# Kernel optimization log

Hardware: AMD Instinct MI355X
Metric: run time of the kernel (lower is better)

Reference implementation:

```python
import jax, jax.numpy as jnp
import numpy as np

KDIM = 2048
RATE = 0.99

def _l2norm(v, axis=1, eps=1e-12):
    n = jnp.linalg.norm(v, axis=axis, keepdims=True)
    return v / jnp.maximum(n, eps)

def _conv3d(x, w, b, stride, pad):
    # x: (N,C,D,H,W), w: (O,I,kd,kh,kw)
    out = jax.lax.conv_general_dilated(
        x, w, window_strides=stride, padding=pad,
        dimension_numbers=('NCDHW', 'OIDHW', 'NCDHW'))
    return out + b[None, :, None, None, None]

def _linear(x, w, b):
    # torch Linear convention: w (out,in)
    return x @ w.T + b

def _memory_block(x, m):
    # x: (n, 400), m: (k, 400)
    k = m.shape[0]
    xn = _l2norm(x)
    mn = _l2norm(m)
    score = xn @ mn.T                                  # (n, k)
    # --- EMA codebook update (fully detached) ---
    xd = jax.lax.stop_gradient(x)
    ind = jnp.argmax(score, axis=1)                    # (n,)
    onehot_sum = jax.ops.segment_sum(jnp.ones(x.shape[0], x.dtype), ind, num_segments=k)
    embed_sum = jax.ops.segment_sum(xd, ind, num_segments=k).T   # (c, k)
    embed_mean = embed_sum / (onehot_sum + 1e-6)                 # (c, k)
    ss = embed_mean.sum(axis=1, keepdims=True)                   # (c, 1)
    param_div = (embed_mean - ss) * 2.0 / k / (k - 1)
    m_new = jax.lax.stop_gradient(m * RATE + (embed_mean + param_div).T * (1.0 - RATE))
    # --- recompute score with updated codebook ---
    mn = _l2norm(m_new)
    score = xn @ mn.T
    out = score @ m_new                                 # (n, c)
    tend = jnp.linalg.norm(out, axis=1)
    tend_1 = jnp.linalg.norm(x, axis=1)
    param = (tend_1 / tend)[:, None]
    out = (param * score) @ m_new
    return out, score


def setup_inputs() -> dict:
    key = jax.random.key(0)
    ks = jax.random.split(key, 24)
    f32 = jnp.float32
    def rn(k, shape, scale):
        return jax.random.normal(k, shape, dtype=f32) * scale
    b = 2048
    inp = {
        'x': rn(ks[0], (b, 1, 200, 5, 5), 1.0),
        'conv1_w': rn(ks[1], (20, 1, 3, 3, 3), 0.2),   'conv1_b': jnp.zeros((20,), f32),
        'pool1_w': rn(ks[2], (20, 20, 3, 1, 1), 0.1),  'pool1_b': jnp.zeros((20,), f32),
        'conv2_w': rn(ks[3], (35, 20, 3, 3, 3), 0.05), 'conv2_b': jnp.zeros((35,), f32),
        'pool2_w': rn(ks[4], (35, 35, 3, 1, 1), 0.1),  'pool2_b': jnp.zeros((35,), f32),
        'conv3_w': rn(ks[5], (35, 35, 3, 1, 1), 0.1),  'conv3_b': jnp.zeros((35,), f32),
        'conv4_w': rn(ks[6], (35, 35, 2, 1, 1), 0.1),  'conv4_b': jnp.zeros((35,), f32),
        'feat_w':  rn(ks[7], (400, 910), 0.03),        'feat_b': jnp.zeros((400,), f32),
        'feat1_w': rn(ks[8], (400, 400), 0.05),        'feat1_b': jnp.zeros((400,), f32),
        'mem_units': rn(ks[9], (KDIM, 400), 1.0),
        'up_w':    rn(ks[10], (400, 400), 0.05),       'up_b': jnp.zeros((400,), f32),
        'cls_w':   rn(ks[11], (16, 400), 0.05),        'cls_b': jnp.zeros((16,), f32),
    }
    return inp


def reference(x, conv1_w, conv1_b, pool1_w, pool1_b, conv2_w, conv2_b,
              pool2_w, pool2_b, conv3_w, conv3_b, conv4_w, conv4_b,
              feat_w, feat_b, feat1_w, feat1_b, mem_units,
              up_w, up_b, cls_w, cls_b):
    h = jax.nn.relu(_conv3d(x, conv1_w, conv1_b, (1, 1, 1), [(0, 0), (0, 0), (0, 0)]))
    h = _conv3d(h, pool1_w, pool1_b, (2, 1, 1), [(1, 1), (0, 0), (0, 0)])
    h = jax.nn.relu(_conv3d(h, conv2_w, conv2_b, (1, 1, 1), [(1, 1), (0, 0), (0, 0)]))
    h = _conv3d(h, pool2_w, pool2_b, (2, 1, 1), [(1, 1), (0, 0), (0, 0)])
    h = jax.nn.relu(_conv3d(h, conv3_w, conv3_b, (1, 1, 1), [(1, 1), (0, 0), (0, 0)]))
    h = jax.nn.relu(_conv3d(h, conv4_w, conv4_b, (2, 1, 1), [(1, 1), (0, 0), (0, 0)]))
    h = h.reshape(h.shape[0], -1)                 # (b, 910)
    fea = _linear(h, feat_w, feat_b)              # (b, 400)
    xx = _linear(fea, feat1_w, feat1_b)           # (b, 400)
    mem_out, _score = _memory_block(xx, jax.lax.stop_gradient(mem_units))
    up = _linear(mem_out, up_w, up_b)
    out_feature = fea - up
    logits = _linear(out_feature, cls_w, cls_b)   # (b, 16)
    return logits
```

## Files before the change

kernel.cpp:

```cpp
#include <hip/hip_runtime.h>

#define BLK 256

constexpr int BB   = 2048;
constexpr int CH2  = 512;
constexpr int NCH2 = BB / CH2;
constexpr int KD   = 2048;
constexpr int CD   = 400;

__global__ __launch_bounds__(256) void fused12_k(const float* __restrict__ x,
                                                 const float* __restrict__ c1w,
                                                 const float* __restrict__ c1b,
                                                 const float* __restrict__ p1w,
                                                 const float* __restrict__ p1b,
                                                 float* __restrict__ h2c, int b0) {
    int bi = blockIdx.x;
    int o0 = blockIdx.y * 17;
    int ocnt = 99 - o0; if (ocnt > 17) ocnt = 17;
    __shared__ float xs[37 * 25];
    __shared__ float c1[20][35][9];
    __shared__ float w1s[540];
    __shared__ float wps[1200];
    __shared__ float b1s[20], bps[20];
    int tid = threadIdx.x;
    for (int i = tid; i < 540; i += 256) w1s[i] = c1w[i];
    for (int i = tid; i < 1200; i += 256) wps[i] = p1w[i];
    if (tid < 20) { b1s[tid] = c1b[tid]; bps[tid] = p1b[tid]; }
    const float* xb = x + (size_t)(b0 + bi) * 5000;
    int r0 = 2 * o0 - 1;
    for (int i = tid; i < 37 * 25; i += 256) {
        int r = r0 + i / 25;
        xs[i] = (r >= 0 && r < 200) ? xb[r * 25 + (i % 25)] : 0.f;
    }
    __syncthreads();
    for (int it = tid; it < 35 * 5; it += 256) {
        int ri = it / 5, g = it % 5;
        int oc0 = g * 4;
        int r = r0 + ri;
        float acc[4][9];
        if (r >= 0 && r <= 197) {
#pragma unroll
            for (int o = 0; o < 4; ++o)
#pragma unroll
                for (int j = 0; j < 9; ++j) acc[o][j] = b1s[oc0 + o];
#pragma unroll
            for (int kd = 0; kd < 3; ++kd) {
                float xv[25];
                const float* xr = &xs[(ri + kd) * 25];
#pragma unroll
                for (int m = 0; m < 25; ++m) xv[m] = xr[m];
#pragma unroll
                for (int o = 0; o < 4; ++o) {
                    const float* wp1 = &w1s[(oc0 + o) * 27 + kd * 9];
#pragma unroll
                    for (int kh = 0; kh < 3; ++kh)
#pragma unroll
                        for (int kw = 0; kw < 3; ++kw) {
                            float w = wp1[kh * 3 + kw];
#pragma unroll
                            for (int oh = 0; oh < 3; ++oh)
#pragma unroll
                                for (int ow = 0; ow < 3; ++ow)
                                    acc[o][oh * 3 + ow] += xv[(oh + kh) * 5 + ow + kw] * w;
                        }
                }
            }
#pragma unroll
            for (int o = 0; o < 4; ++o)
#pragma unroll
                for (int j = 0; j < 9; ++j) c1[oc0 + o][ri][j] = fmaxf(acc[o][j], 0.f);
        } else {
#pragma unroll
            for (int o = 0; o < 4; ++o)
#pragma unroll
                for (int j = 0; j < 9; ++j) c1[oc0 + o][ri][j] = 0.f;
        }
    }
    __syncthreads();
    for (int it = tid; it < ocnt * 5; it += 256) {
        int oi = it / 5, g = it % 5;
        int oc0 = g * 4;
        float acc[4][9];
#pragma unroll
        for (int o = 0; o < 4; ++o)
#pragma unroll
            for (int j = 0; j < 9; ++j) acc[o][j] = bps[oc0 + o];
        for (int ic = 0; ic < 20; ++ic) {
            float win[3][9];
#pragma unroll
            for (int kd = 0; kd < 3; ++kd)
#pragma unroll
                for (int j = 0; j < 9; ++j) win[kd][j] = c1[ic][2 * oi + kd][j];
#pragma unroll
            for (int o = 0; o < 4; ++o) {
                const float* wp = &wps[((oc0 + o) * 20 + ic) * 3];
#pragma unroll
                for (int kd = 0; kd < 3; ++kd) {
                    float w = wp[kd];
#pragma unroll
                    for (int j = 0; j < 9; ++j) acc[o][j] += win[kd][j] * w;
                }
            }
        }
#pragma unroll
        for (int o = 0; o < 4; ++o) {
            float* ou = h2c + (((size_t)bi * 20 + (oc0 + o)) * 99 + (o0 + oi)) * 9;
#pragma unroll
            for (int j = 0; j < 9; ++j) ou[j] = acc[o][j];
        }
    }
}

__global__ __launch_bounds__(512) void conv2b_k(const float* __restrict__ h2c,
                                                const float* __restrict__ w,
                                                const float* __restrict__ bias,
                                                float* __restrict__ h3, int b0) {
    int bi = blockIdx.x;
    __shared__ float h2s[10][101][9];
    __shared__ float ws[35 * 271];
    int tid = threadIdx.x;
    int oc = tid % 35, run = tid / 35;
    int od_start = run * 7;
    bool active = tid < 490;
    float acc[8];
    float bv = active ? bias[oc] : 0.f;
#pragma unroll
    for (int i = 0; i < 8; ++i) acc[i] = bv;
    const float* src = h2c + (size_t)bi * 17820;
    for (int s = 0; s < 2; ++s) {
        for (int i = tid; i < 10 * 9; i += 512) {
            int ic = i / 9, j = i % 9;
            h2s[ic][0][j] = 0.f; h2s[ic][100][j] = 0.f;
        }
        for (int i = tid; i < 8910; i += 512) {
            int ic = i / 891;
            ((float*)h2s)[i + ic * 18 + 9] = src[s * 8910 + i];
        }
        for (int i = tid; i < 35 * 270; i += 512) {
            int o = i / 270, t = i % 270;
            ws[o * 271 + t] = w[(size_t)o * 540 + s * 270 + t];
        }
        __syncthreads();
        if (active) {
            const float* wp = &ws[oc * 271];
            for (int ic = 0; ic < 10; ++ic) {
#pragma unroll
                for (int j = 0; j < 9; ++j) {
                    float win[10];
#pragma unroll
                    for (int t = 0; t < 10; ++t) win[t] = h2s[ic][od_start + t][j];
#pragma unroll
                    for (int kd = 0; kd < 3; ++kd) {
                        float wv = wp[(ic * 3 + kd) * 9 + j];
#pragma unroll
                        for (int i = 0; i < 8; ++i) acc[i] += win[i + kd] * wv;
                    }
                }
            }
        }
        __syncthreads();
    }
    if (active) {
        float* o = h3 + ((size_t)(b0 + bi) * 35 + oc) * 99 + od_start;
#pragma unroll
        for (int i = 0; i < 8; ++i) o[i] = fmaxf(acc[i], 0.f);
    }
}

__global__ __launch_bounds__(256) void fused345_k(const float* __restrict__ h3,
                                                  const float* __restrict__ w2, const float* __restrict__ b2,
                                                  const float* __restrict__ w3, const float* __restrict__ b3,
                                                  const float* __restrict__ w4, const float* __restrict__ b4,
                                                  float* __restrict__ h6) {
    int b = blockIdx.x;
    __shared__ float h3s[35][101];
    __shared__ float h4s[35][53];
    __shared__ float h5s[35][53];
    __shared__ float wbuf[3675];
    __shared__ float bbuf[35];
    int tid = threadIdx.x;
    int oc = tid % 35, run = tid / 35;
    bool act = tid < 245;
    for (int i = tid; i < 35; i += 256) {
        h3s[i][0] = 0.f; h3s[i][100] = 0.f;
        h4s[i][0] = 0.f; h4s[i][51] = 0.f;
        h5s[i][0] = 0.f; h5s[i][51] = 0.f;
    }
    for (int i = tid; i < 35 * 99; i += 256) h3s[i / 99][1 + i % 99] = h3[(size_t)b * 3465 + i];
    for (int i = tid; i < 3675; i += 256) wbuf[i] = w2[i];
    if (tid < 35) bbuf[tid] = b2[tid];
    __syncthreads();
    if (act) {
        int od0 = run * 7;
        float acc[8];
        float bv = bbuf[oc];
#pragma unroll
        for (int i = 0; i < 8; ++i) acc[i] = bv;
        const float* wrow = &wbuf[oc * 105];
        for (int ic = 0; ic < 35; ++ic) {
            float w0 = wrow[ic * 3], w1 = wrow[ic * 3 + 1], w2v = wrow[ic * 3 + 2];
            float win[17];
#pragma unroll
            for (int t = 0; t < 17; ++t) win[t] = h3s[ic][2 * od0 + t];
#pragma unroll
            for (int i = 0; i < 8; ++i)
                acc[i] += win[2 * i] * w0 + win[2 * i + 1] * w1 + win[2 * i + 2] * w2v;
        }
#pragma unroll
        for (int i = 0; i < 8; ++i) h4s[oc][1 + od0 + i] = acc[i];
    }
    __syncthreads();
    for (int i = tid; i < 3675; i += 256) wbuf[i] = w3[i];
    if (tid < 35) bbuf[tid] = b3[tid];
    __syncthreads();
    if (act) {
        int od0 = run * 7;
        float acc[8];
        float bv = bbuf[oc];
#pragma unroll
        for (int i = 0; i < 8; ++i) acc[i] = bv;
        const float* wrow = &wbuf[oc * 105];
        for (int ic = 0; ic < 35; ++ic) {
            float w0 = wrow[ic * 3], w1 = wrow[ic * 3 + 1], w2v = wrow[ic * 3 + 2];
            float win[10];
#pragma unroll
            for (int t = 0; t < 10; ++t) win[t] = h4s[ic][od0 + t];
#pragma unroll
            for (int i = 0; i < 8; ++i)
                acc[i] += win[i] * w0 + win[i + 1] * w1 + win[i + 2] * w2v;
        }
#pragma unroll
        for (int i = 0; i < 8; ++i) h5s[oc][1 + od0 + i] = fmaxf(acc[i], 0.f);
    }
    __syncthreads();
    for (int i = tid; i < 2450; i += 256) wbuf[i] = w4[i];
    if (tid < 35) bbuf[tid] = b4[tid];
    __syncthreads();
    if (act) {
        int od0 = run * 4; if (od0 > 22) od0 = 22;
        float acc[4];
        float bv = bbuf[oc];
#pragma unroll
        for (int i = 0; i < 4; ++i) acc[i] = bv;
        const float* wrow = &wbuf[oc * 70];
        for (int ic = 0; ic < 35; ++ic) {
            float w0 = wrow[ic * 2], w1 = wrow[ic * 2 + 1];
            float win[8];
#pragma unroll
            for (int t = 0; t < 8; ++t) win[t] = h5s[ic][2 * od0 + t];
#pragma unroll
            for (int i = 0; i < 4; ++i)
                acc[i] += win[2 * i] * w0 + win[2 * i + 1] * w1;
        }
#pragma unroll
        for (int i = 0; i < 4; ++i) {
            int od = od0 + i;
            if (od < 26) h6[(size_t)b * 910 + oc * 26 + od] = fmaxf(acc[i], 0.f);
        }
    }
}

template <int BM, int BN, int TM, int TN, bool GUARD, bool ARGMAX, bool SPLITK>
__global__ __launch_bounds__(256) void gemm_nt(const float* __restrict__ A,
                                               const float* __restrict__ B,
                                               const float* __restrict__ bias,
                                               float* __restrict__ C,
                                               const float* __restrict__ colscale,
                                               unsigned long long* __restrict__ keymax,
                                               int M, int N, int K) {
    constexpr int BK = 16;
    constexpr int AI = BM / 16, BI = BN / 16;
    __shared__ float As[BK][BM + 4];
    __shared__ float Bs[BK][BN + 4];
    int tid = threadIdx.x;
    int tx = tid % (BN / TN), ty = tid / (BN / TN);
    int row0 = blockIdx.y * BM;
    int col0 = blockIdx.x * BN;
    int kbase = 0, kend = K;
    if constexpr (SPLITK) {
        int nz = gridDim.z;
        int kchunk = (((K + nz - 1) / nz) + BK - 1) / BK * BK;
        kbase = blockIdx.z * kchunk;
        kend = kbase + kchunk;
        if (kend > K) kend = K;
    }
    int kk = tid % 16, ld = tid / 16;
    float ra[AI], rb[BI];
    auto loadA = [&](int k0, float* r) {
        int gk = k0 + kk;
#pragma unroll
        for (int i = 0; i < AI; ++i) {
            int gr = row0 + ld + 16 * i;
            float v = 0.f;
            if ((!GUARD && !SPLITK) || (gr < M && gk < kend)) v = A[(size_t)gr * K + gk];
            r[i] = v;
        }
    };
    auto loadB = [&](int k0, float* r) {
        int gk = k0 + kk;
#pragma unroll
        for (int i = 0; i < BI; ++i) {
            int gn = col0 + ld + 16 * i;
            float v = 0.f;
            if ((!GUARD && !SPLITK) || (gn < N && gk < kend)) v = B[(size_t)gn * K + gk];
            r[i] = v;
        }
    };
    auto stash = [&]() {
#pragma unroll
        for (int i = 0; i < AI; ++i) As[kk][ld + 16 * i] = ra[i];
#pragma unroll
        for (int i = 0; i < BI; ++i) Bs[kk][ld + 16 * i] = rb[i];
    };
    float acc[TM][TN] = {};
    int nt = (kend - kbase + BK - 1) / BK;
    loadA(kbase, ra); loadB(kbase, rb);
    stash();
    __syncthreads();
    for (int t = 0; t < nt; ++t) {
        bool more = (t + 1 < nt);
        if (more) { loadA(kbase + (t + 1) * BK, ra); loadB(kbase + (t + 1) * BK, rb); }
#pragma unroll
        for (int k = 0; k < BK; ++k) {
            float a[TM], b[TN];
            *(float4*)&a[0] = *(const float4*)&As[k][ty * TM];
            if constexpr (TM == 8) *(float4*)&a[4] = *(const float4*)&As[k][ty * TM + 4];
            *(float4*)&b[0] = *(const float4*)&Bs[k][tx * TN];
            if constexpr (TN == 8) *(float4*)&b[4] = *(const float4*)&Bs[k][tx * TN + 4];
#pragma unroll
            for (int i = 0; i < TM; ++i)
#pragma unroll
                for (int j = 0; j < TN; ++j) acc[i][j] += a[i] * b[j];
        }
        if (more) {
            __syncthreads();
            stash();
            __syncthreads();
        }
    }
    if constexpr (ARGMAX) {
        __shared__ unsigned long long red[BM][17];
#pragma unroll
        for (int i = 0; i < TM; ++i) {
            unsigned long long best = 0;
#pragma unroll
            for (int j = 0; j < TN; ++j) {
                int gc = col0 + tx * TN + j;
                float v = acc[i][j] * colscale[gc];
                unsigned u = __float_as_uint(v);
                unsigned ukey = (u & 0x80000000u) ? ~u : (u | 0x80000000u);
                unsigned long long key =
                    ((unsigned long long)ukey << 32) | (unsigned)(N - 1 - gc);
                if (key > best) best = key;
            }
            red[ty * TM + i][tx] = best;
        }
        __syncthreads();
        if (tid < BM) {
            unsigned long long best = 0;
#pragma unroll
            for (int q = 0; q < 16; ++q) {
                unsigned long long v = red[tid][q];
                if (v > best) best = v;
            }
            atomicMax(&keymax[row0 + tid], best);
        }
    } else {
#pragma unroll
        for (int i = 0; i < TM; ++i) {
            int gr = row0 + ty * TM + i;
            if (GUARD && gr >= M) continue;
#pragma unroll
            for (int j = 0; j < TN; ++j) {
                int gc = col0 + tx * TN + j;
                if (GUARD && gc >= N) continue;
                float v = acc[i][j];
                if constexpr (SPLITK) {
                    if (bias && blockIdx.z == 0) v += bias[gc];
                    atomicAdd(&C[(size_t)gr * N + gc], v);
                } else {
                    if (bias) v += bias[gc];
                    C[(size_t)gr * N + gc] = v;
                }
            }
        }
    }
}

__global__ __launch_bounds__(256) void gemm_tn_g(const float* __restrict__ mnew,
                                                 const float* __restrict__ nrm2,
                                                 float* __restrict__ G, int kchunk) {
    constexpr int BK = 16;
    __shared__ float As[BK][64];
    __shared__ float Bs[BK][64];
    int tid = threadIdx.x;
    int tx = tid % 16, ty = tid / 16;
    int c0 = blockIdx.y * 64, d0 = blockIdx.x * 64;
    int kbase = blockIdx.z * kchunk;
    int cl = tid % 64, kk0 = tid / 64;
    int gc0 = c0 + cl, gd0 = d0 + cl;
    bool cok = gc0 < CD, dok = gd0 < CD;
    float pa[4], pb[4];
    auto ld = [&](int k0) {
#pragma unroll
        for (int i = 0; i < 4; ++i) {
            int gk = k0 + kk0 + 4 * i;
            float s = 1.0f / fmaxf(nrm2[gk], 1e-12f);
            pa[i] = cok ? mnew[(size_t)gk * CD + gc0] * s : 0.f;
            pb[i] = dok ? mnew[(size_t)gk * CD + gd0] : 0.f;
        }
    };
    auto stash = [&]() {
#pragma unroll
        for (int i = 0; i < 4; ++i) {
            As[kk0 + 4 * i][cl] = pa[i];
            Bs[kk0 + 4 * i][cl] = pb[i];
        }
    };
    float acc[4][4] = {};
    int nt = kchunk / BK;
    ld(kbase); stash(); __syncthreads();
    for (int t = 0; t < nt; ++t) {
        bool more = (t + 1 < nt);
        if (more) ld(kbase + (t + 1) * BK);
#pragma unroll
        for (int k = 0; k < BK; ++k) {
            float a[4], b[4];
            *(float4*)&a[0] = *(const float4*)&As[k][ty * 4];
            *(float4*)&b[0] = *(const float4*)&Bs[k][tx * 4];
#pragma unroll
            for (int i = 0; i < 4; ++i)
#pragma unroll
                for (int j = 0; j < 4; ++j) acc[i][j] += a[i] * b[j];
        }
        if (more) { __syncthreads(); stash(); __syncthreads(); }
    }
#pragma unroll
    for (int i = 0; i < 4; ++i) {
        int gc = c0 + ty * 4 + i;
        if (gc >= CD) continue;
#pragma unroll
        for (int j = 0; j < 4; ++j) {
            int gd = d0 + tx * 4 + j;
            if (gd >= CD) continue;
            atomicAdd(&G[(size_t)gc * CD + gd], acc[i][j]);
        }
    }
}


__global__ __launch_bounds__(BLK) void rownorm_k(const float* __restrict__ in,
                                                 float* __restrict__ nrm, int rows, int cols) {
    int row  = blockIdx.x * (BLK / 64) + ((int)threadIdx.x / 64);
    int lane = threadIdx.x & 63;
    if (row >= rows) return;
    const float* p = in + (size_t)row * cols;
    float s = 0.f;
    for (int c = lane; c < cols; c += 64) { float v = p[c]; s += v * v; }
#pragma unroll
    for (int off = 32; off; off >>= 1) s += __shfl_down(s, off);
    if (lane == 0) nrm[row] = sqrtf(s);
}

__global__ __launch_bounds__(BLK) void scatter_k(const float* __restrict__ xx,
                                                 const unsigned long long* __restrict__ kb,
                                                 float* __restrict__ esum,
                                                 float* __restrict__ counts) {
    int idx = blockIdx.x * BLK + threadIdx.x;
    if (idx >= BB * CD) return;
    int n = idx / CD, c = idx % CD;
    int k = (KD - 1) - (int)(unsigned)(kb[n] & 0xffffffffull);
    atomicAdd(&esum[(size_t)k * CD + c], xx[idx]);
    if (c == 0) atomicAdd(&counts[k], 1.0f);
}

__global__ __launch_bounds__(BLK) void ss2_k(const float* __restrict__ esum,
                                             const float* __restrict__ counts,
                                             float* __restrict__ ss) {
    int k0 = blockIdx.x * 8;
    int tid = threadIdx.x;
    float a0 = 0.f, a1 = 0.f;
    for (int r = 0; r < 8; ++r) {
        int k = k0 + r;
        float rc = 1.0f / (counts[k] + 1e-6f);
        a0 += esum[(size_t)k * CD + tid] * rc;
        if (tid < CD - BLK) a1 += esum[(size_t)k * CD + BLK + tid] * rc;
    }
    atomicAdd(&ss[tid], a0);
    if (tid < CD - BLK) atomicAdd(&ss[BLK + tid], a1);
}

__global__ __launch_bounds__(BLK) void mnew_k(const float* __restrict__ m,
                                              const float* __restrict__ esum,
                                              const float* __restrict__ counts,
                                              const float* __restrict__ ss,
                                              float* __restrict__ mnew) {
    int idx = blockIdx.x * BLK + threadIdx.x;
    if (idx >= KD * CD) return;
    int k = idx / CD, c = idx % CD;
    float mean = esum[idx] / (counts[k] + 1e-6f);
    float pd = (mean - ss[c]) * (2.0f / ((float)KD * (float)(KD - 1)));
    mnew[idx] = m[idx] * 0.99f + (mean + pd) * 0.01f;
}

__global__ __launch_bounds__(BLK) void q_k(const float* __restrict__ cls_w,
                                           const float* __restrict__ up_w,
                                           float* __restrict__ Q) {
    int idx = blockIdx.x * BLK + threadIdx.x;
    if (idx >= 16 * CD) return;
    int o = idx / CD, c = idx % CD;
    float s = 0.f;
    for (int i = 0; i < CD; ++i) s += cls_w[o * CD + i] * up_w[(size_t)i * CD + c];
    Q[idx] = s;
}

__global__ __launch_bounds__(64) void bias2_k(const float* __restrict__ cls_w,
                                              const float* __restrict__ up_b,
                                              const float* __restrict__ cls_b,
                                              float* __restrict__ bias2) {
    int o = threadIdx.x;
    if (o >= 16) return;
    float s = 0.f;
    for (int i = 0; i < CD; ++i) s += up_b[i] * cls_w[o * CD + i];
    bias2[o] = cls_b[o] - s;
}

__global__ __launch_bounds__(BLK) void cls2_k(const float* __restrict__ fea,
                                              const float* __restrict__ Y,
                                              const float* __restrict__ t1,
                                              const float* __restrict__ u,
                                              const float* __restrict__ cls_w,
                                              const float* __restrict__ Q,
                                              const float* __restrict__ bias2,
                                              float* __restrict__ out) {
    int t = blockIdx.x * BLK + threadIdx.x;
    if (t >= BB * 16) return;
    int o = t % 16, b = t / 16;
    float rs = t1[b] / u[b];
    const float* fp = fea + (size_t)b * CD;
    const float* yp = Y + (size_t)b * CD;
    const float* cw = cls_w + o * CD;
    const float* qp = Q + o * CD;
    float a1 = 0.f, a2 = 0.f;
    for (int i = 0; i < CD; ++i) { a1 += fp[i] * cw[i]; a2 += yp[i] * qp[i]; }
    out[t] = bias2[o] + a1 - rs * a2;
}


static inline int cdiv(int a, int b) { return (a + b - 1) / b; }

extern "C" void kernel_launch(void* const* d_in, const int* in_sizes, int n_in,
                              void* d_out, int out_size, void* d_ws, size_t ws_size,
                              hipStream_t stream) {
    const float* x       = (const float*)d_in[0];
    const float* conv1_w = (const float*)d_in[1];
    const float* conv1_b = (const float*)d_in[2];
    const float* pool1_w = (const float*)d_in[3];
    const float* pool1_b = (const float*)d_in[4];
    const float* conv2_w = (const float*)d_in[5];
    const float* conv2_b = (const float*)d_in[6];
    const float* pool2_w = (const float*)d_in[7];
    const float* pool2_b = (const float*)d_in[8];
    const float* conv3_w = (const float*)d_in[9];
    const float* conv3_b = (const float*)d_in[10];
    const float* conv4_w = (const float*)d_in[11];
    const float* conv4_b = (const float*)d_in[12];
    const float* feat_w  = (const float*)d_in[13];
    const float* feat_b  = (const float*)d_in[14];
    const float* feat1_w = (const float*)d_in[15];
    const float* feat1_b = (const float*)d_in[16];
    const float* mem     = (const float*)d_in[17];
    const float* up_w    = (const float*)d_in[18];
    const float* up_b    = (const float*)d_in[19];
    const float* cls_w   = (const float*)d_in[20];
    const float* cls_b   = (const float*)d_in[21];
    float* outp = (float*)d_out;

    float* ws = (float*)d_ws;
    size_t off = 0;
    auto alloc = [&](size_t n) { float* p = ws + off; off += n; return p; };

    unsigned long long* keybuf = (unsigned long long*)alloc(2 * BB);
    float* h2c   = alloc((size_t)CH2 * 17820);
    float* h3    = alloc((size_t)BB * 35 * 99);
    float* h6    = alloc((size_t)BB * 910);
    float* fea   = alloc((size_t)BB * CD);
    float* xx    = alloc((size_t)BB * CD);
    float* Y     = alloc((size_t)BB * CD);
    float* counts= alloc(KD);
    float* esum  = alloc((size_t)KD * CD);
    float* ssb   = alloc(CD);
    float* mnewb = alloc((size_t)KD * CD);
    float* G     = alloc((size_t)CD * CD);
    float* t1    = alloc(BB);
    float* u     = alloc(BB);
    float* Q     = alloc((size_t)16 * CD);
    float* bias2 = alloc(16);
    float* mnrm  = alloc(KD);
    float* nrm2  = alloc(KD);

    hipMemsetAsync(keybuf, 0, BB * sizeof(unsigned long long), stream);
    hipMemsetAsync(counts, 0, (KD + (size_t)KD * CD + CD) * sizeof(float), stream);
    hipMemsetAsync(fea, 0, (size_t)3 * BB * CD * sizeof(float), stream);
    hipMemsetAsync(G, 0, (size_t)CD * CD * sizeof(float), stream);

    q_k<<<cdiv(16 * CD, BLK), BLK, 0, stream>>>(cls_w, up_w, Q);
    bias2_k<<<1, 64, 0, stream>>>(cls_w, up_b, cls_b, bias2);
    rownorm_k<<<cdiv(KD, 4), BLK, 0, stream>>>(mem, mnrm, KD, CD);

    for (int ch = 0; ch < NCH2; ++ch) {
        int b0 = ch * CH2;
        dim3 g12(CH2, 6);
        fused12_k<<<g12, 256, 0, stream>>>(x, conv1_w, conv1_b, pool1_w, pool1_b, h2c, b0);
        conv2b_k<<<CH2, 512, 0, stream>>>(h2c, conv2_w, conv2_b, h3, b0);
    }
    fused345_k<<<BB, 256, 0, stream>>>(h3, pool2_w, pool2_b, conv3_w, conv3_b,
                                       conv4_w, conv4_b, h6);

    {
        dim3 g(cdiv(CD, 64), BB / 64, 2);
        gemm_nt<64, 64, 4, 4, true, false, true><<<g, 256, 0, stream>>>(
            h6, feat_w, feat_b, fea, nullptr, nullptr, BB, CD, 910);
        gemm_nt<64, 64, 4, 4, true, false, true><<<g, 256, 0, stream>>>(
            fea, feat1_w, feat1_b, xx, nullptr, nullptr, BB, CD, CD);
    }

    rownorm_k<<<cdiv(BB, 4), BLK, 0, stream>>>(xx, t1, BB, CD);

    {
        dim3 g(KD / 128, BB / 128);
        gemm_nt<128, 128, 8, 8, false, true, false><<<g, 256, 0, stream>>>(
            xx, mem, nullptr, nullptr, mnrm, keybuf, BB, KD, CD);
    }
    scatter_k<<<cdiv(BB * CD, BLK), BLK, 0, stream>>>(xx, keybuf, esum, counts);
    ss2_k<<<KD / 8, BLK, 0, stream>>>(esum, counts, ssb);
    mnew_k<<<cdiv(KD * CD, BLK), BLK, 0, stream>>>(mem, esum, counts, ssb, mnewb);

    rownorm_k<<<cdiv(KD, 4), BLK, 0, stream>>>(mnewb, nrm2, KD, CD);

    {
        dim3 g(cdiv(CD, 64), cdiv(CD, 64), 8);
        gemm_tn_g<<<g, 256, 0, stream>>>(mnewb, nrm2, G, KD / 8);
    }
    {
        dim3 g(cdiv(CD, 64), BB / 64, 2);
        gemm_nt<64, 64, 4, 4, true, false, true><<<g, 256, 0, stream>>>(
            xx, G, nullptr, Y, nullptr, nullptr, BB, CD, CD);
    }
    rownorm_k<<<cdiv(BB, 4), BLK, 0, stream>>>(Y, u, BB, CD);

    cls2_k<<<cdiv(BB * 16, BLK), BLK, 0, stream>>>(fea, Y, t1, u, cls_w, Q, bias2, outp);
}
```

Before: 1.012 ms.

## Restructure conv2 to two output channels per thread with smaller LDS stages

The conv2 kernel now runs 256 threads per block, and each thread computes two output channels. Input channels are streamed in four stages of 5 instead of two stages of 10. This shrinks shared memory per block and reuses each loaded input window across two weights, so more blocks can be resident and fewer LDS reads are needed per FMA. The fused345 kernel also aliases its h5 buffer onto h3s to cut LDS footprint. The cost is more barriers per block and higher register pressure from the doubled accumulators.

New measurement: 942.7 us. 1.07x faster.

```diff
diff --git a/kernel.cpp b/kernel.cpp
--- a/kernel.cpp
+++ b/kernel.cpp
@@ -111,39 +111,46 @@
     }
 }
 
-__global__ __launch_bounds__(512) void conv2b_k(const float* __restrict__ h2c,
+__global__ __launch_bounds__(256) void conv2b_k(const float* __restrict__ h2c,
                                                 const float* __restrict__ w,
                                                 const float* __restrict__ bias,
                                                 float* __restrict__ h3, int b0) {
     int bi = blockIdx.x;
-    __shared__ float h2s[10][101][9];
-    __shared__ float ws[35 * 271];
+    __shared__ float h2s[5][101][9];
+    __shared__ float ws[36 * 137];
     int tid = threadIdx.x;
-    int oc = tid % 35, run = tid / 35;
+    int g = tid % 18, run = tid / 18;
+    int oc0 = g * 2;
     int od_start = run * 7;
-    bool active = tid < 490;
-    float acc[8];
-    float bv = active ? bias[oc] : 0.f;
-#pragma unroll
-    for (int i = 0; i < 8; ++i) acc[i] = bv;
+    bool active = tid < 252;
+    float acc[2][8];
+    float bv0 = 0.f, bv1 = 0.f;
+    if (active) {
+        bv0 = bias[oc0];
+        bv1 = (oc0 + 1 < 35) ? bias[oc0 + 1] : 0.f;
+    }
+#pragma unroll
+    for (int i = 0; i < 8; ++i) { acc[0][i] = bv0; acc[1][i] = bv1; }
     const float* src = h2c + (size_t)bi * 17820;
-    for (int s = 0; s < 2; ++s) {
-        for (int i = tid; i < 10 * 9; i += 512) {
+    for (int s = 0; s < 4; ++s) {
+        for (int i = tid; i < 5 * 9; i += 256) {
             int ic = i / 9, j = i % 9;
             h2s[ic][0][j] = 0.f; h2s[ic][100][j] = 0.f;
         }
-        for (int i = tid; i < 8910; i += 512) {
+        for (int i = tid; i < 4455; i += 256) {
             int ic = i / 891;
-            ((float*)h2s)[i + ic * 18 + 9] = src[s * 8910 + i];
-        }
-        for (int i = tid; i < 35 * 270; i += 512) {
-            int o = i / 270, t = i % 270;
-            ws[o * 271 + t] = w[(size_t)o * 540 + s * 270 + t];
-        }
+            ((float*)h2s)[i + ic * 18 + 9] = src[s * 4455 + i];
+        }
+        for (int i = tid; i < 35 * 135; i += 256) {
+            int o = i / 135, t = i % 135;
+            ws[o * 137 + t] = w[(size_t)o * 540 + s * 135 + t];
+        }
+        for (int i = tid; i < 137; i += 256) ws[35 * 137 + i] = 0.f;
         __syncthreads();
         if (active) {
-            const float* wp = &ws[oc * 271];
-            for (int ic = 0; ic < 10; ++ic) {
+            const float* wp0 = &ws[oc0 * 137];
+            const float* wp1 = &ws[(oc0 + 1) * 137];
+            for (int ic = 0; ic < 5; ++ic) {
 #pragma unroll
                 for (int j = 0; j < 9; ++j) {
                     float win[10];
@@ -151,9 +158,13 @@
                     for (int t = 0; t < 10; ++t) win[t] = h2s[ic][od_start + t][j];
 #pragma unroll
                     for (int kd = 0; kd < 3; ++kd) {
-                        float wv = wp[(ic * 3 + kd) * 9 + j];
-#pragma unroll
-                        for (int i = 0; i < 8; ++i) acc[i] += win[i + kd] * wv;
+                        float wv0 = wp0[(ic * 3 + kd) * 9 + j];
+                        float wv1 = wp1[(ic * 3 + kd) * 9 + j];
+#pragma unroll
+                        for (int i = 0; i < 8; ++i) {
+                            acc[0][i] += win[i + kd] * wv0;
+                            acc[1][i] += win[i + kd] * wv1;
+                        }
                     }
                 }
             }
@@ -161,9 +172,15 @@
         __syncthreads();
     }
     if (active) {
-        float* o = h3 + ((size_t)(b0 + bi) * 35 + oc) * 99 + od_start;
-#pragma unroll
-        for (int i = 0; i < 8; ++i) o[i] = fmaxf(acc[i], 0.f);
+#pragma unroll
+        for (int o = 0; o < 2; ++o) {
+            int oc = oc0 + o;
+            if (oc < 35) {
+                float* ou = h3 + ((size_t)(b0 + bi) * 35 + oc) * 99 + od_start;
+#pragma unroll
+                for (int i = 0; i < 8; ++i) ou[i] = fmaxf(acc[o][i], 0.f);
+            }
+        }
     }
 }
 
@@ -175,16 +192,15 @@
     int b = blockIdx.x;
     __shared__ float h3s[35][101];
     __shared__ float h4s[35][53];
-    __shared__ float h5s[35][53];
     __shared__ float wbuf[3675];
     __shared__ float bbuf[35];
+    float (*h5s)[101] = h3s;
     int tid = threadIdx.x;
     int oc = tid % 35, run = tid / 35;
     bool act = tid < 245;
     for (int i = tid; i < 35; i += 256) {
         h3s[i][0] = 0.f; h3s[i][100] = 0.f;
-        h4s[i][0] = 0.f; h4s[i][51] = 0.f;
-        h5s[i][0] = 0.f; h5s[i][51] = 0.f;
+        h4s[i][0] = 0.f; h4s[i][51] = 0.f; h4s[i][52] = 0.f;
     }
     for (int i = tid; i < 35 * 99; i += 256) h3s[i / 99][1 + i % 99] = h3[(size_t)b * 3465 + i];
     for (int i = tid; i < 3675; i += 256) wbuf[i] = w2[i];
@@ -212,6 +228,7 @@
     __syncthreads();
     for (int i = tid; i < 3675; i += 256) wbuf[i] = w3[i];
     if (tid < 35) bbuf[tid] = b3[tid];
+    for (int i = tid; i < 35; i += 256) { h5s[i][0] = 0.f; h5s[i][51] = 0.f; }
     __syncthreads();
     if (act) {
         int od0 = run * 7;
@@ -612,7 +629,7 @@
         int b0 = ch * CH2;
         dim3 g12(CH2, 6);
         fused12_k<<<g12, 256, 0, stream>>>(x, conv1_w, conv1_b, pool1_w, pool1_b, h2c, b0);
-        conv2b_k<<<CH2, 512, 0, stream>>>(h2c, conv2_w, conv2_b, h3, b0);
+        conv2b_k<<<CH2, 256, 0, stream>>>(h2c, conv2_w, conv2_b, h3, b0);
     }
     fused345_k<<<BB, 256, 0, stream>>>(h3, pool2_w, pool2_b, conv3_w, conv3_b,
                                        conv4_w, conv4_b, h6);
```
